# Kernel tuning notes

Measured on AMD Instinct MI355X. Metric: run time of the kernel, lower is better.

Reference implementation:

```python
import jax, jax.numpy as jnp
import numpy as np

WEIGHT_ENERGY = 0.1
WEIGHT_COV = 0.005
EPS = 1e-9
COV_EPS = 1e-6
TWO_PI = 2.0 * np.pi


def setup_inputs() -> dict:
    key = jax.random.key(0)
    k1, k2 = jax.random.split(key)
    z = jax.random.normal(k1, (16, 256, 64, 32), dtype=jnp.float32)
    gamma = jax.random.uniform(k2, (16, 256, 64, 8), dtype=jnp.float32)
    return {"z": z, "gamma": gamma}


def _gmm_loss(z, gamma):
    # z: [B,T,F,D], gamma: [B,T,F,K]
    D = z.shape[-1]
    N = z.shape[0] * z.shape[1] * z.shape[2]
    sum_gamma = jnp.sum(gamma, axis=(0, 1, 2))            # [K]
    phi = sum_gamma / N                                    # [K]
    mu = jnp.einsum('btfk,btfd->kd', gamma, z) / sum_gamma[:, None]  # [K,D]
    z_mu = z[..., None, :] - mu                            # [B,T,F,K,D]
    # covariance per component (gamma-weighted outer products)
    cov = jnp.einsum('btfk,btfkd,btfke->kde', gamma, z_mu, z_mu) / sum_gamma[:, None, None]
    eye = jnp.eye(D, dtype=z.dtype)
    cov = cov + CO_EPS_I(eye)
    cov_k = cov + EPS * eye                                # [K,D,D]
    cov_inv = jnp.linalg.inv(cov_k)                        # [K,D,D]
    L = jnp.linalg.cholesky(cov_k * TWO_PI)                # [K,D,D]
    det_cov = jnp.prod(jnp.diagonal(L, axis1=-2, axis2=-1), axis=-1)  # [K] (= sqrt(det(2pi*cov)))
    cov_diag = jnp.sum(1.0 / jnp.diagonal(cov_k, axis1=-2, axis2=-1))
    # quadratic-form energy, fused reduction over D
    E_z = -0.5 * jnp.einsum('btfkd,kde,btfke->btfk', z_mu, cov_inv, z_mu)
    E_z = jnp.exp(E_z)
    E_z = -jnp.log(jnp.sum(phi * E_z / jnp.sqrt(det_cov), axis=-1) + COV_EPS)
    sample_energy = jnp.mean(E_z)
    sample_energy = jnp.where(jnp.isfinite(sample_energy), sample_energy, 0.0)
    cov_diag = jnp.where(jnp.isfinite(cov_diag), cov_diag, 0.0)
    return WEIGHT_ENERGY * sample_energy + WEIGHT_COV * cov_diag


def CO_EPS_I(eye):
    return COV_EPS * eye


def reference(z, gamma):
    return _gmm_loss(z, gamma)
```

## Files before the change

### kernel.cpp

```cpp
#include <hip/hip_runtime.h>
#include <math.h>

#define NS (16*256*64)
#define D 32
#define K 8

typedef __attribute__((ext_vector_type(8))) short bf16x8;
typedef __attribute__((ext_vector_type(16))) float f32x16;

#define WS_ENERGY   0
#define WS_COVDIAG  1
#define WS_C        16
#define WS_COEF     24
#define WS_SG       32
#define WS_S1       64
#define WS_S2       1024
#define WS_FRAGA    9216
#define WS_FRAGB    13312
#define WS_PART     16384
#define PART_STRIDE 8456

__device__ __forceinline__ short f2bf(float f) {
    union { float f; unsigned u; } v; v.f = f;
    unsigned r = v.u + 0x7FFFu + ((v.u >> 16) & 1u);
    return (short)(r >> 16);
}

__global__ __launch_bounds__(256) void k_moments(const float* __restrict__ z,
                                                 const float* __restrict__ g,
                                                 float* __restrict__ part) {
    __shared__ float zs[64][32];
    __shared__ float gs[64][8];
    const int t   = threadIdx.x;
    const int w   = t >> 6;
    const int l   = t & 63;
    const int col = l & 31;
    const int nh  = l >> 5;
    const int k0  = 2 * w;

    f32x16 acc0 = {}; f32x16 acc1 = {};
    float s1a = 0.f, s1b = 0.f, sga = 0.f, sgb = 0.f;

    for (int c = blockIdx.x; c < NS / 64; c += gridDim.x) {
        const int base = c * 64;
        __syncthreads();
        const float4* zsrc = (const float4*)(z + (size_t)base * 32);
        float4* zdst = (float4*)(&zs[0][0]);
        zdst[t]       = zsrc[t];
        zdst[t + 256] = zsrc[t + 256];
        if (t < 128) {
            ((float4*)(&gs[0][0]))[t] = ((const float4*)(g + (size_t)base * 8))[t];
        }
        __syncthreads();
#pragma unroll
        for (int sc = 0; sc < 4; sc++) {
            const int s0 = sc * 16 + nh * 8;
            float zf[8], ga[8], gb[8];
#pragma unroll
            for (int j = 0; j < 8; j++) {
                zf[j] = zs[s0 + j][col];
                float2 gg = *(const float2*)(&gs[s0 + j][k0]);
                ga[j] = gg.x; gb[j] = gg.y;
            }
            bf16x8 af, b0, b1;
#pragma unroll
            for (int j = 0; j < 8; j++) {
                float p0 = ga[j] * zf[j];
                float p1 = gb[j] * zf[j];
                af[j] = f2bf(zf[j]);
                b0[j] = f2bf(p0);
                b1[j] = f2bf(p1);
                s1a += p0;  s1b += p1;
                sga += ga[j];  sgb += gb[j];
            }
            acc0 = __builtin_amdgcn_mfma_f32_32x32x16_bf16(af, b0, acc0, 0, 0, 0);
            acc1 = __builtin_amdgcn_mfma_f32_32x32x16_bf16(af, b1, acc1, 0, 0, 0);
        }
    }
    s1a += __shfl_xor(s1a, 32);  s1b += __shfl_xor(s1b, 32);
    sga += __shfl_xor(sga, 32);  sgb += __shfl_xor(sgb, 32);

    float* pb = part + (size_t)blockIdx.x * PART_STRIDE;
#pragma unroll
    for (int r = 0; r < 16; r++) {
        int row = (r & 3) + 8 * (r >> 2) + 4 * nh;
        pb[(size_t)k0 * 1024 + row * 32 + col]       = acc0[r];
        pb[(size_t)(k0 + 1) * 1024 + row * 32 + col] = acc1[r];
    }
    if (l < 32) {
        pb[8192 + k0 * 32 + col]       = s1a;
        pb[8192 + (k0 + 1) * 32 + col] = s1b;
    }
    if (l == 0) { pb[8448 + k0] = sga; pb[8448 + k0 + 1] = sgb; }
}

__global__ __launch_bounds__(1024) void k_reduce(float* __restrict__ ws, int nblk) {
    __shared__ float red[16][64];
    const int t  = threadIdx.x;
    const int el = t & 63;
    const int bg = t >> 6;
    const int e  = blockIdx.x * 64 + el;
    const float* part = ws + WS_PART;
    float s = 0.0f;
    if (e < PART_STRIDE) {
        for (int b = bg; b < nblk; b += 16)
            s += part[(size_t)b * PART_STRIDE + e];
    }
    red[bg][el] = s;
    __syncthreads();
#pragma unroll
    for (int h = 8; h > 0; h >>= 1) {
        if (bg < h) red[bg][el] += red[bg + h][el];
        __syncthreads();
    }
    if (bg == 0 && e < PART_STRIDE) {
        float v = red[0][el];
        if (e < 8192)       ws[WS_S2 + e] = v;
        else if (e < 8448)  ws[WS_S1 + (e - 8192)] = v;
        else                ws[WS_SG + (e - 8448)] = v;
    }
    if (blockIdx.x == 0) {
        if (t < 512) ws[WS_FRAGB + t] = 0.0f;
        if (t == 0) { ws[WS_ENERGY] = 0.0f; ws[WS_COVDIAG] = 0.0f; }
    }
}

__global__ __launch_bounds__(64) void k_prep(float* __restrict__ ws) {
    __shared__ float Am[32][33];
    __shared__ float mus[32];
    __shared__ float bLs[32];

    const int k   = blockIdx.x;
    const int l   = threadIdx.x;
    const int c32 = l & 31;
    const bool right = l >= 32;

    const float sgk = ws[WS_SG + k];
    if (l < 32) mus[l] = ws[WS_S1 + k * 32 + l] / sgk;
    __syncthreads();
    const float mc  = mus[c32];
    const float rsg = 1.0f / sgk;

    float x[32];
    float dval = 1.0f;
#pragma unroll
    for (int r = 0; r < 32; r++) {
        float v;
        if (right) {
            v = (r == c32) ? 1.0f : 0.0f;
        } else {
            v = ws[WS_S2 + k * 1024 + r * 32 + c32] * rsg - mus[r] * mc;
            if (r == c32) { v += 1.0e-6f + 1.0e-9f; dval = v; }
        }
        x[r] = v;
    }

    {
        float tdi = right ? 0.0f : 1.0f / dval;
#pragma unroll
        for (int m = 1; m < 64; m <<= 1) tdi += __shfl_xor(tdi, m);
        if (l == 0) atomicAdd(&ws[WS_COVDIAG], tdi);
    }

    float logdet = 0.0f;
#pragma unroll
    for (int j = 0; j < 32; j++) {
        float piv = __shfl(x[j], j);
        float rp  = 1.0f / piv;
        logdet += __logf(piv);
        x[j] *= rp;
#pragma unroll
        for (int r = 0; r < 32; r++) {
            if (r == j) continue;
            float m = __shfl(x[r], j);
            x[r] -= m * x[j];
        }
    }
    if (right) {
#pragma unroll
        for (int r = 0; r < 32; r++) Am[r][c32] = x[r];
    }
    __syncthreads();

    if (l == 0) {
        float phi = sgk / (float)NS;
        ws[WS_COEF + k] = phi * __expf(-(8.0f * 1.8378770664093453f + 0.25f * logdet));
    }

    if (l < 32) {
        float s = 0.0f;
#pragma unroll
        for (int c = 0; c < 32; c++) s += Am[c32][c] * mus[c];
        bLs[c32] = s;
    }
    __syncthreads();
    {
        float cm = (l < 32) ? mus[c32] * bLs[c32] : 0.0f;
#pragma unroll
        for (int m = 1; m < 64; m <<= 1) cm += __shfl_xor(cm, m);
        if (l == 0) ws[WS_C + k] = cm;
    }

    {
        const int ph = l >> 5;
#pragma unroll
        for (int h = 0; h < 2; h++) {
            int r = c32, cb = ph * 8 + 16 * h;
            unsigned uu[4];
#pragma unroll
            for (int q = 0; q < 4; q++) {
                unsigned lo2 = (unsigned short)f2bf(Am[r][cb + 2 * q]);
                unsigned hi2 = (unsigned short)f2bf(Am[r][cb + 2 * q + 1]);
                uu[q] = lo2 | (hi2 << 16);
            }
            ((uint4*)(ws + WS_FRAGA))[(k * 2 + h) * 64 + l] = make_uint4(uu[0], uu[1], uu[2], uu[3]);
        }
        if (c32 == k) {
#pragma unroll
            for (int h = 0; h < 2; h++) {
                int cb = ph * 8 + 16 * h;
                unsigned uu[4];
#pragma unroll
                for (int q = 0; q < 4; q++) {
                    unsigned lo2 = (unsigned short)f2bf(bLs[cb + 2 * q]);
                    unsigned hi2 = (unsigned short)f2bf(bLs[cb + 2 * q + 1]);
                    uu[q] = lo2 | (hi2 << 16);
                }
                ((uint4*)(ws + WS_FRAGB))[h * 64 + l] = make_uint4(uu[0], uu[1], uu[2], uu[3]);
            }
        }
    }
}

__global__ __launch_bounds__(512) void k_energy(const float* __restrict__ z,
                                                float* __restrict__ ws) {
    __shared__ uint4 frg[1152];
    __shared__ float red[512];
    const int t   = threadIdx.x;
    const int w   = t >> 6;
    const int l   = t & 63;
    const int col = l & 31;
    const int nh  = l >> 5;

    for (int i = t; i < 1152; i += 512) frg[i] = ((const uint4*)(ws + WS_FRAGA))[i];
    float cf[8], cc[8];
#pragma unroll
    for (int k = 0; k < 8; k++) { cf[k] = ws[WS_COEF + k]; cc[k] = ws[WS_C + k]; }
    __syncthreads();

    float En = 0.0f;
    for (int ci = 0; ci < 2; ci++) {
        const int chunk = (blockIdx.x * 8 + w) * 2 + ci;
        const int n0 = chunk * 32;
        const float* zb = z + (size_t)(n0 + col) * 32 + nh * 8;
        float4 a0 = *(const float4*)(zb + 0);
        float4 a1 = *(const float4*)(zb + 4);
        float4 a2 = *(const float4*)(zb + 16);
        float4 a3 = *(const float4*)(zb + 20);
        float zlo[8] = {a0.x,a0.y,a0.z,a0.w,a1.x,a1.y,a1.z,a1.w};
        float zhi[8] = {a2.x,a2.y,a2.z,a2.w,a3.x,a3.y,a3.z,a3.w};
        bf16x8 b0, b1;
#pragma unroll
        for (int j = 0; j < 8; j++) { b0[j] = f2bf(zlo[j]); b1[j] = f2bf(zhi[j]); }
        float olo[4], ohi[4];
#pragma unroll
        for (int j = 0; j < 4; j++) {
            float mlo = nh ? zlo[j] : zlo[j + 4];
            float mhi = nh ? zhi[j] : zhi[j + 4];
            olo[j] = __shfl_xor(mlo, 32);
            ohi[j] = __shfl_xor(mhi, 32);
        }
        float zdot[16];
#pragma unroll
        for (int j = 0; j < 4; j++) {
            zdot[j]      = nh ? olo[j]     : zlo[j];
            zdot[4 + j]  = nh ? zlo[4 + j] : olo[j];
            zdot[8 + j]  = nh ? ohi[j]     : zhi[j];
            zdot[12 + j] = nh ? zhi[4 + j] : ohi[j];
        }
        f32x16 acc2 = {};
        {
            bf16x8 fb0 = *(const bf16x8*)&frg[1024 + l];
            bf16x8 fb1 = *(const bf16x8*)&frg[1024 + 64 + l];
            acc2 = __builtin_amdgcn_mfma_f32_32x32x16_bf16(fb0, b0, acc2, 0, 0, 0);
            acc2 = __builtin_amdgcn_mfma_f32_32x32x16_bf16(fb1, b1, acc2, 0, 0, 0);
        }
        float oth[4];
#pragma unroll
        for (int r = 0; r < 4; r++) oth[r] = __shfl_xor(acc2[r], 32);
        float pk[8];
#pragma unroll
        for (int k = 0; k < 8; k++) {
            bf16x8 fa0 = *(const bf16x8*)&frg[(k * 2 + 0) * 64 + l];
            bf16x8 fa1 = *(const bf16x8*)&frg[(k * 2 + 1) * 64 + l];
            f32x16 acc = {};
            acc = __builtin_amdgcn_mfma_f32_32x32x16_bf16(fa0, b0, acc, 0, 0, 0);
            acc = __builtin_amdgcn_mfma_f32_32x32x16_bf16(fa1, b1, acc, 0, 0, 0);
            float p = 0.0f;
#pragma unroll
            for (int r = 0; r < 16; r++) p += acc[r] * zdot[r];
            p += __shfl_xor(p, 32);
            pk[k] = p;
        }
        float ssum = 0.0f;
#pragma unroll
        for (int k = 0; k < 8; k++) {
            float d2 = (k < 4) ? (nh ? oth[k] : acc2[k]) : (nh ? acc2[k - 4] : oth[k - 4]);
            float E = pk[k] - 2.0f * d2 + cc[k];
            ssum += cf[k] * __expf(-0.5f * E);
        }
        En += -__logf(ssum + 1.0e-6f);
    }
    red[t] = En;
    __syncthreads();
    for (int s2 = 256; s2 > 0; s2 >>= 1) { if (t < s2) red[t] += red[t + s2]; __syncthreads(); }
    if (t == 0) atomicAdd(&ws[WS_ENERGY], red[0]);
}

__global__ void k_final(const float* __restrict__ ws, float* __restrict__ out) {
    float se = ws[WS_ENERGY] * 0.5f / (float)NS;
    if (!isfinite(se)) se = 0.0f;
    float cd = ws[WS_COVDIAG];
    if (!isfinite(cd)) cd = 0.0f;
    out[0] = 0.1f * se + 0.005f * cd;
}

extern "C" void kernel_launch(void* const* d_in, const int* in_sizes, int n_in,
                              void* d_out, int out_size, void* d_ws, size_t ws_size,
                              hipStream_t stream) {
    const float* z = (const float*)d_in[0];
    const float* g = (const float*)d_in[1];
    float* out = (float*)d_out;
    float* ws  = (float*)d_ws;

    long avail = (long)(ws_size / 4) - WS_PART;
    int nblk = (int)(avail / PART_STRIDE);
    if (nblk > 512) nblk = 512;
    if (nblk < 1)   nblk = 1;

    k_moments<<<nblk, 256, 0, stream>>>(z, g, ws + WS_PART);
    k_reduce<<<(PART_STRIDE + 63) / 64, 1024, 0, stream>>>(ws, nblk);
    k_prep<<<8, 64, 0, stream>>>(ws);
    k_energy<<<512, 512, 0, stream>>>(z, ws);
    k_final<<<1, 1, 0, stream>>>(ws, out);
}
```

Measured before the change: 79.79 us.

## Use hardware bf16 conversion, MFMA row sums, and fuse final into energy kernel

Replaces the manual round-to-nearest bf16 conversion with vectorized __bf16 convertvector, which should map to native packed-convert instructions. In the moments kernel, the gamma-weighted first moments are now computed by extra MFMAs against a ones vector, and gamma sums are accumulated from the vector loads and combined with shared atomics. The per-lane scalar accumulations are removed. The energy kernel now uses a wave-shuffle reduction instead of a shared-memory tree, and a last-block-done counter computes the final output in place of a separate k_final launch. The trade-offs are two extra MFMAs per step, with the first moments now accumulated from bf16-rounded products, and reliance on atomic ordering for the final write.

```diff
diff --git a/kernel.cpp b/kernel.cpp
--- a/kernel.cpp
+++ b/kernel.cpp
@@ -1,4 +1,5 @@
 #include <hip/hip_runtime.h>
+#include <hip/hip_bf16.h>
 #include <math.h>
 
 #define NS (16*256*64)
@@ -6,10 +7,13 @@
 #define K 8
 
 typedef __attribute__((ext_vector_type(8))) short bf16x8;
+typedef __attribute__((ext_vector_type(8))) float f32x8;
+typedef __attribute__((ext_vector_type(8))) __bf16 bf16v8;
 typedef __attribute__((ext_vector_type(16))) float f32x16;
 
 #define WS_ENERGY   0
 #define WS_COVDIAG  1
+#define WS_DONE     2
 #define WS_C        16
 #define WS_COEF     24
 #define WS_SG       32
@@ -20,10 +24,15 @@
 #define WS_PART     16384
 #define PART_STRIDE 8456
 
-__device__ __forceinline__ short f2bf(float f) {
-    union { float f; unsigned u; } v; v.f = f;
-    unsigned r = v.u + 0x7FFFu + ((v.u >> 16) & 1u);
-    return (short)(r >> 16);
+__device__ __forceinline__ bf16x8 cvt8(f32x8 v) {
+    union { bf16v8 h; bf16x8 s; } u;
+    u.h = __builtin_convertvector(v, bf16v8);
+    return u.s;
+}
+__device__ __forceinline__ short f2bf1(float f) {
+    union { __bf16 h; short s; } u;
+    u.h = (__bf16)f;
+    return u.s;
 }
 
 __global__ __launch_bounds__(256) void k_moments(const float* __restrict__ z,
@@ -31,6 +40,7 @@
                                                  float* __restrict__ part) {
     __shared__ float zs[64][32];
     __shared__ float gs[64][8];
+    __shared__ float sgs[8];
     const int t   = threadIdx.x;
     const int w   = t >> 6;
     const int l   = t & 63;
@@ -38,8 +48,12 @@
     const int nh  = l >> 5;
     const int k0  = 2 * w;
 
-    f32x16 acc0 = {}; f32x16 acc1 = {};
-    float s1a = 0.f, s1b = 0.f, sga = 0.f, sgb = 0.f;
+    f32x16 acc0 = {}, acc1 = {}, accA = {}, accB = {};
+    float sg4[4] = {0.f, 0.f, 0.f, 0.f};
+    bf16x8 ones;
+#pragma unroll
+    for (int j = 0; j < 8; j++) ones[j] = (short)0x3F80;
+    if (t < 8) sgs[t] = 0.0f;
 
     for (int c = blockIdx.x; c < NS / 64; c += gridDim.x) {
         const int base = c * 64;
@@ -49,36 +63,35 @@
         zdst[t]       = zsrc[t];
         zdst[t + 256] = zsrc[t + 256];
         if (t < 128) {
-            ((float4*)(&gs[0][0]))[t] = ((const float4*)(g + (size_t)base * 8))[t];
+            float4 gv = ((const float4*)(g + (size_t)base * 8))[t];
+            ((float4*)(&gs[0][0]))[t] = gv;
+            sg4[0] += gv.x; sg4[1] += gv.y; sg4[2] += gv.z; sg4[3] += gv.w;
         }
         __syncthreads();
 #pragma unroll
         for (int sc = 0; sc < 4; sc++) {
             const int s0 = sc * 16 + nh * 8;
-            float zf[8], ga[8], gb[8];
+            f32x8 zv, p0, p1;
 #pragma unroll
             for (int j = 0; j < 8; j++) {
-                zf[j] = zs[s0 + j][col];
+                float zf = zs[s0 + j][col];
                 float2 gg = *(const float2*)(&gs[s0 + j][k0]);
-                ga[j] = gg.x; gb[j] = gg.y;
+                zv[j] = zf;
+                p0[j] = gg.x * zf;
+                p1[j] = gg.y * zf;
             }
-            bf16x8 af, b0, b1;
-#pragma unroll
-            for (int j = 0; j < 8; j++) {
-                float p0 = ga[j] * zf[j];
-                float p1 = gb[j] * zf[j];
-                af[j] = f2bf(zf[j]);
-                b0[j] = f2bf(p0);
-                b1[j] = f2bf(p1);
-                s1a += p0;  s1b += p1;
-                sga += ga[j];  sgb += gb[j];
-            }
-            acc0 = __builtin_amdgcn_mfma_f32_32x32x16_bf16(af, b0, acc0, 0, 0, 0);
-            acc1 = __builtin_amdgcn_mfma_f32_32x32x16_bf16(af, b1, acc1, 0, 0, 0);
-        }
-    }
-    s1a += __shfl_xor(s1a, 32);  s1b += __shfl_xor(s1b, 32);
-    sga += __shfl_xor(sga, 32);  sgb += __shfl_xor(sgb, 32);
+            bf16x8 af = cvt8(zv), b0 = cvt8(p0), b1 = cvt8(p1);
+            acc0 = __builtin_amdgcn_mfma_f32_32x32x16_bf16(af,   b0, acc0, 0, 0, 0);
+            acc1 = __builtin_amdgcn_mfma_f32_32x32x16_bf16(af,   b1, acc1, 0, 0, 0);
+            accA = __builtin_amdgcn_mfma_f32_32x32x16_bf16(ones, b0, accA, 0, 0, 0);
+            accB = __builtin_amdgcn_mfma_f32_32x32x16_bf16(ones, b1, accB, 0, 0, 0);
+        }
+    }
+    __syncthreads();
+    if (t < 128) {
+#pragma unroll
+        for (int q = 0; q < 4; q++) atomicAdd(&sgs[4 * (t & 1) + q], sg4[q]);
+    }
 
     float* pb = part + (size_t)blockIdx.x * PART_STRIDE;
 #pragma unroll
@@ -87,11 +100,12 @@
         pb[(size_t)k0 * 1024 + row * 32 + col]       = acc0[r];
         pb[(size_t)(k0 + 1) * 1024 + row * 32 + col] = acc1[r];
     }
-    if (l < 32) {
-        pb[8192 + k0 * 32 + col]       = s1a;
-        pb[8192 + (k0 + 1) * 32 + col] = s1b;
-    }
-    if (l == 0) { pb[8448 + k0] = sga; pb[8448 + k0 + 1] = sgb; }
+    if (nh == 0) {
+        pb[8192 + k0 * 32 + col]       = accA[0];
+        pb[8192 + (k0 + 1) * 32 + col] = accB[0];
+    }
+    __syncthreads();
+    if (t < 8) pb[8448 + t] = sgs[t];
 }
 
 __global__ __launch_bounds__(1024) void k_reduce(float* __restrict__ ws, int nblk) {
@@ -121,7 +135,11 @@
     }
     if (blockIdx.x == 0) {
         if (t < 512) ws[WS_FRAGB + t] = 0.0f;
-        if (t == 0) { ws[WS_ENERGY] = 0.0f; ws[WS_COVDIAG] = 0.0f; }
+        if (t == 0) {
+            ws[WS_ENERGY] = 0.0f;
+            ws[WS_COVDIAG] = 0.0f;
+            ((unsigned*)ws)[WS_DONE] = 0u;
+        }
     }
 }
 
@@ -209,8 +227,8 @@
             unsigned uu[4];
 #pragma unroll
             for (int q = 0; q < 4; q++) {
-                unsigned lo2 = (unsigned short)f2bf(Am[r][cb + 2 * q]);
-                unsigned hi2 = (unsigned short)f2bf(Am[r][cb + 2 * q + 1]);
+                unsigned lo2 = (unsigned short)f2bf1(Am[r][cb + 2 * q]);
+                unsigned hi2 = (unsigned short)f2bf1(Am[r][cb + 2 * q + 1]);
                 uu[q] = lo2 | (hi2 << 16);
             }
             ((uint4*)(ws + WS_FRAGA))[(k * 2 + h) * 64 + l] = make_uint4(uu[0], uu[1], uu[2], uu[3]);
@@ -222,8 +240,8 @@
                 unsigned uu[4];
 #pragma unroll
                 for (int q = 0; q < 4; q++) {
-                    unsigned lo2 = (unsigned short)f2bf(bLs[cb + 2 * q]);
-                    unsigned hi2 = (unsigned short)f2bf(bLs[cb + 2 * q + 1]);
+                    unsigned lo2 = (unsigned short)f2bf1(bLs[cb + 2 * q]);
+                    unsigned hi2 = (unsigned short)f2bf1(bLs[cb + 2 * q + 1]);
                     uu[q] = lo2 | (hi2 << 16);
                 }
                 ((uint4*)(ws + WS_FRAGB))[h * 64 + l] = make_uint4(uu[0], uu[1], uu[2], uu[3]);
@@ -233,9 +251,10 @@
 }
 
 __global__ __launch_bounds__(512) void k_energy(const float* __restrict__ z,
-                                                float* __restrict__ ws) {
+                                                float* __restrict__ ws,
+                                                float* __restrict__ out) {
     __shared__ uint4 frg[1152];
-    __shared__ float red[512];
+    __shared__ float redw[8];
     const int t   = threadIdx.x;
     const int w   = t >> 6;
     const int l   = t & 63;
@@ -257,11 +276,9 @@
         float4 a1 = *(const float4*)(zb + 4);
         float4 a2 = *(const float4*)(zb + 16);
         float4 a3 = *(const float4*)(zb + 20);
-        float zlo[8] = {a0.x,a0.y,a0.z,a0.w,a1.x,a1.y,a1.z,a1.w};
-        float zhi[8] = {a2.x,a2.y,a2.z,a2.w,a3.x,a3.y,a3.z,a3.w};
-        bf16x8 b0, b1;
-#pragma unroll
-        for (int j = 0; j < 8; j++) { b0[j] = f2bf(zlo[j]); b1[j] = f2bf(zhi[j]); }
+        f32x8 zlo = {a0.x,a0.y,a0.z,a0.w,a1.x,a1.y,a1.z,a1.w};
+        f32x8 zhi = {a2.x,a2.y,a2.z,a2.w,a3.x,a3.y,a3.z,a3.w};
+        bf16x8 b0 = cvt8(zlo), b1 = cvt8(zhi);
         float olo[4], ohi[4];
 #pragma unroll
         for (int j = 0; j < 4; j++) {
@@ -311,18 +328,26 @@
         }
         En += -__logf(ssum + 1.0e-6f);
     }
-    red[t] = En;
-    __syncthreads();
-    for (int s2 = 256; s2 > 0; s2 >>= 1) { if (t < s2) red[t] += red[t + s2]; __syncthreads(); }
-    if (t == 0) atomicAdd(&ws[WS_ENERGY], red[0]);
-}
-
-__global__ void k_final(const float* __restrict__ ws, float* __restrict__ out) {
-    float se = ws[WS_ENERGY] * 0.5f / (float)NS;
-    if (!isfinite(se)) se = 0.0f;
-    float cd = ws[WS_COVDIAG];
-    if (!isfinite(cd)) cd = 0.0f;
-    out[0] = 0.1f * se + 0.005f * cd;
+#pragma unroll
+    for (int m = 1; m < 64; m <<= 1) En += __shfl_xor(En, m);
+    if (l == 0) redw[w] = En;
+    __syncthreads();
+    if (t == 0) {
+        float s = 0.0f;
+#pragma unroll
+        for (int i = 0; i < 8; i++) s += redw[i];
+        atomicAdd(&ws[WS_ENERGY], s);
+        __threadfence();
+        unsigned old = atomicAdd((unsigned*)ws + WS_DONE, 1u);
+        if (old == gridDim.x - 1) {
+            float se = atomicAdd(&ws[WS_ENERGY], 0.0f);
+            se = se * 0.5f / (float)NS;
+            if (!isfinite(se)) se = 0.0f;
+            float cd = ws[WS_COVDIAG];
+            if (!isfinite(cd)) cd = 0.0f;
+            out[0] = 0.1f * se + 0.005f * cd;
+        }
+    }
 }
 
 extern "C" void kernel_launch(void* const* d_in, const int* in_sizes, int n_in,
@@ -341,6 +366,5 @@
     k_moments<<<nblk, 256, 0, stream>>>(z, g, ws + WS_PART);
     k_reduce<<<(PART_STRIDE + 63) / 64, 1024, 0, stream>>>(ws, nblk);
     k_prep<<<8, 64, 0, stream>>>(ws);
-    k_energy<<<512, 512, 0, stream>>>(z, ws);
-    k_final<<<1, 1, 0, stream>>>(ws, out);
-}
+    k_energy<<<512, 512, 0, stream>>>(z, ws, out);
+}
```

Measured after the change: 82.47 us. 3.4% more time.
